# Kernel optimization log

Hardware: AMD Instinct MI355X
Metric: run time of the kernel (lower is better)

## Reference

```python
import jax, jax.numpy as jnp
import numpy as np

NUM_BUCKETS = 320
MAX_DISTANCE = 800


def _layer_norm(x, w, b, eps=1e-5):
    x32 = x.astype(jnp.float32)
    mu = x32.mean(-1, keepdims=True)
    var = x32.var(-1, keepdims=True)
    return ((x32 - mu) / jnp.sqrt(var + eps) * w + b).astype(x.dtype)


def _rel_pos_bucket(rel):
    half = NUM_BUCKETS // 2            # 160
    st = half // 2                     # 80 (small threshold)
    sign = (rel >= 0).astype(jnp.int32)
    ab = jnp.abs(rel)
    is_small = ab < st
    log_ratio = jnp.log(jnp.clip(ab.astype(jnp.float32), 1.0) / st) / np.float32(np.log(MAX_DISTANCE / st))
    log_pos = st + (log_ratio * (half - st)).astype(jnp.int32)  # trunc toward zero like .long()
    log_pos = jnp.minimum(log_pos, half - 1)
    bucket = jnp.where(is_small, ab, log_pos) + sign * half
    return jnp.clip(bucket, 0, NUM_BUCKETS - 1)


def setup_inputs() -> dict:
    key = jax.random.key(0)
    B, T, C, H, FF = 2, 2048, 768, 12, 3072
    D = C // H
    ks = jax.random.split(key, 16)
    s = 0.02
    return {
        "x": jax.random.normal(ks[0], (B, T, C), jnp.float32),
        "ln1_w": jnp.ones((C,), jnp.float32),
        "ln1_b": jnp.zeros((C,), jnp.float32),
        "wq": jax.random.normal(ks[1], (C, C), jnp.float32) * s,
        "bq": jnp.zeros((C,), jnp.float32),
        "wk": jax.random.normal(ks[2], (C, C), jnp.float32) * s,
        "bk": jnp.zeros((C,), jnp.float32),
        "wv": jax.random.normal(ks[3], (C, C), jnp.float32) * s,
        "bv": jnp.zeros((C,), jnp.float32),
        "wo": jax.random.normal(ks[4], (C, C), jnp.float32) * s,
        "bo": jnp.zeros((C,), jnp.float32),
        "ln2_w": jnp.ones((C,), jnp.float32),
        "ln2_b": jnp.zeros((C,), jnp.float32),
        "w1": jax.random.normal(ks[5], (FF, C), jnp.float32) * s,
        "b1": jnp.zeros((FF,), jnp.float32),
        "w2": jax.random.normal(ks[6], (C, FF), jnp.float32) * s,
        "b2": jnp.zeros((C,), jnp.float32),
        "rel_embed": jax.random.normal(ks[7], (NUM_BUCKETS, H), jnp.float32),
        "gate_ur_w": jax.random.normal(ks[8], (H, D), jnp.float32) * 0.01,
        "gate_i_w": jax.random.normal(ks[9], (H, D), jnp.float32) * 0.01,
        "rel_scale": jnp.ones((H,), jnp.float32),
    }


def reference(x, ln1_w, ln1_b, wq, bq, wk, bk, wv, bv, wo, bo,
              ln2_w, ln2_b, w1, b1, w2, b2, rel_embed, gate_ur_w, gate_i_w, rel_scale):
    B, T, C = x.shape
    H = rel_embed.shape[1]
    D = C // H

    residual = x
    h = _layer_norm(x, ln1_w, ln1_b)
    q = (h @ wq.T + bq).reshape(B, T, H, D).transpose(0, 2, 1, 3)  # [B,H,T,D]
    k = (h @ wk.T + bk).reshape(B, T, H, D).transpose(0, 2, 1, 3)
    v = (h @ wv.T + bv).reshape(B, T, H, D).transpose(0, 2, 1, 3)

    attn = jnp.einsum('bhqd,bhkd->bhqk', q, k) * (D ** -0.5)

    # gated relative position bias
    pos = jnp.arange(T)
    rel = pos[None, :] - pos[:, None]                 # [T,T]
    buckets = _rel_pos_bucket(rel)                    # [T,T]
    pe = rel_embed[buckets]                           # [T,T,H]
    pe = jnp.transpose(pe, (2, 0, 1))[None]           # [1,H,T,T]
    g_in = q.mean(axis=2).transpose(0, 2, 1).mean(axis=-1)   # [B,D]
    gate_r = jax.nn.sigmoid(g_in @ gate_ur_w.T)       # [B,H]
    gate_u = jax.nn.sigmoid(g_in @ gate_i_w.T)        # [B,H]
    gate = 1.0 + (gate_u * rel_scale[None, :] * gate_r)[:, :, None, None]
    bias = pe * gate                                  # [B,H,T,T]

    attn = jax.nn.softmax(attn + bias, axis=-1)
    out = jnp.einsum('bhqk,bhkd->bhqd', attn, v).transpose(0, 2, 1, 3).reshape(B, T, C)
    x = residual + out @ wo.T + bo

    residual = x
    h = _layer_norm(x, ln2_w, ln2_b)
    h = jax.nn.gelu(h @ w1.T + b1, approximate=False) @ w2.T + b2
    return residual + h
```

## Files before the change

### kernel.cpp

```cpp
#include <hip/hip_runtime.h>
#include <hip/hip_bf16.h>


#define Tn 2048
#define Cn 768
#define Hn 12
#define Dn 64
#define FFn 3072
#define Mn 4096
#define QKVS 2304

typedef __attribute__((ext_vector_type(8))) short bfrag;
typedef __attribute__((ext_vector_type(8))) unsigned short us8;
typedef __attribute__((ext_vector_type(4))) float f32x4;

__device__ __forceinline__ unsigned short f2bu(float f){
  __hip_bfloat16 h = __float2bfloat16(f);
  return *(unsigned short*)&h;
}
__device__ __forceinline__ float bu2f(unsigned short u){
  union { unsigned int i; float f; } v; v.i = ((unsigned int)u) << 16; return v.f;
}
__device__ __forceinline__ us8 pack8(float4 a, float4 b){
  us8 c;
  c[0]=f2bu(a.x); c[1]=f2bu(a.y); c[2]=f2bu(a.z); c[3]=f2bu(a.w);
  c[4]=f2bu(b.x); c[5]=f2bu(b.y); c[6]=f2bu(b.z); c[7]=f2bu(b.w);
  return c;
}

__device__ __forceinline__ float block_reduce_sum(float v, float* sred){
  #pragma unroll
  for (int off = 32; off > 0; off >>= 1) v += __shfl_down(v, off, 64);
  __syncthreads();
  if ((threadIdx.x & 63) == 0) sred[threadIdx.x >> 6] = v;
  __syncthreads();
  return sred[0] + sred[1] + sred[2] + sred[3];
}
__device__ __forceinline__ float rowsum16(float v){
  v += __shfl_xor(v, 1, 16);
  v += __shfl_xor(v, 2, 16);
  v += __shfl_xor(v, 4, 16);
  v += __shfl_xor(v, 8, 16);
  return v;
}

__global__ __launch_bounds__(256) void cast_all_kernel(
    const float* __restrict__ wq, const float* __restrict__ wk,
    const float* __restrict__ wv, const float* __restrict__ wo,
    const float* __restrict__ w1, const float* __restrict__ w2,
    const float* __restrict__ bq, const float* __restrict__ bk,
    const float* __restrict__ bv,
    unsigned short* __restrict__ Wqkv, unsigned short* __restrict__ Wob,
    unsigned short* __restrict__ W1b, unsigned short* __restrict__ W2b,
    float* __restrict__ bqkv)
{
  const int blk = blockIdx.x;
  if (blk >= 3456){
    const int i = (blk - 3456) * 256 + threadIdx.x;
    bqkv[i] = (i < Cn) ? bq[i] : (i < 2 * Cn) ? bk[i - Cn] : bv[i - 2 * Cn];
    return;
  }
  const float* src; unsigned short* dst; int i;
  if (blk < 288)      { src = wq; dst = Wqkv;               i = blk * 256 + threadIdx.x; }
  else if (blk < 576) { src = wk; dst = Wqkv + Cn * Cn;     i = (blk - 288) * 256 + threadIdx.x; }
  else if (blk < 864) { src = wv; dst = Wqkv + 2 * Cn * Cn; i = (blk - 576) * 256 + threadIdx.x; }
  else if (blk < 1152){ src = wo; dst = Wob;                i = (blk - 864) * 256 + threadIdx.x; }
  else if (blk < 2304){ src = w1; dst = W1b;                i = (blk - 1152) * 256 + threadIdx.x; }
  else                { src = w2; dst = W2b;                i = (blk - 2304) * 256 + threadIdx.x; }
  const float4 a = ((const float4*)src)[i * 2];
  const float4 b = ((const float4*)src)[i * 2 + 1];
  *(us8*)&dst[i * 8] = pack8(a, b);
}

__global__ __launch_bounds__(256) void ln_kernel(const float* __restrict__ xin,
    const float* __restrict__ w, const float* __restrict__ bsh,
    unsigned short* __restrict__ out)
{
  __shared__ float xs[Cn];
  __shared__ float sred[4];
  const size_t base = (size_t)blockIdx.x * Cn;
  float s = 0.f;
  for (int c = threadIdx.x; c < Cn; c += 256){
    float v = xin[base + c];
    xs[c] = v; s += v;
  }
  const float mean = block_reduce_sum(s, sred) * (1.f / Cn);
  float s2 = 0.f;
  for (int c = threadIdx.x; c < Cn; c += 256){
    float d = xs[c] - mean; s2 += d * d;
  }
  const float var = block_reduce_sum(s2, sred) * (1.f / Cn);
  const float rstd = rsqrtf(var + 1e-5f);
  for (int c = threadIdx.x; c < Cn; c += 256)
    out[base + c] = f2bu((xs[c] - mean) * rstd * w[c] + bsh[c]);
}

template<int EPI>
__global__ __launch_bounds__(256) void gemm_mfma_kernel(
    const unsigned short* __restrict__ A, const unsigned short* __restrict__ Bw,
    const float* __restrict__ bias, const float* __restrict__ res,
    void* __restrict__ Cout, int M, int N, int K)
{
  __shared__ __align__(16) unsigned short As[128 * 32];
  __shared__ __align__(16) unsigned short Bs[128 * 32];
  const int tid = threadIdx.x;
  const int lane = tid & 63, w = tid >> 6;
  const int nl = lane & 15, quad = lane >> 4;
  const int wm = w >> 1, wn = w & 1;
  const int bm = blockIdx.y * 128, bn = blockIdx.x * 128;
  const int l4 = lane >> 2, lk = (lane & 3) * 8;

  f32x4 acc[4][4];
  #pragma unroll
  for (int i = 0; i < 4; i++)
    #pragma unroll
    for (int j = 0; j < 4; j++) acc[i][j] = (f32x4){0.f, 0.f, 0.f, 0.f};

  const int c0 = w, c1 = w + 4;
  const unsigned short* A0 = A + (size_t)(bm + c0 * 16 + l4) * K + lk;
  const unsigned short* A1 = A + (size_t)(bm + c1 * 16 + l4) * K + lk;
  const unsigned short* B0 = Bw + (size_t)(bn + c0 * 16 + l4) * K + lk;
  const unsigned short* B1 = Bw + (size_t)(bn + c1 * 16 + l4) * K + lk;

  for (int k0 = 0; k0 < K; k0 += 32){
    __syncthreads();
    __builtin_amdgcn_global_load_lds(
        (const __attribute__((address_space(1))) void*)(A0 + k0),
        (__attribute__((address_space(3))) void*)&As[c0 * 512], 16, 0, 0);
    __builtin_amdgcn_global_load_lds(
        (const __attribute__((address_space(1))) void*)(A1 + k0),
        (__attribute__((address_space(3))) void*)&As[c1 * 512], 16, 0, 0);
    __builtin_amdgcn_global_load_lds(
        (const __attribute__((address_space(1))) void*)(B0 + k0),
        (__attribute__((address_space(3))) void*)&Bs[c0 * 512], 16, 0, 0);
    __builtin_amdgcn_global_load_lds(
        (const __attribute__((address_space(1))) void*)(B1 + k0),
        (__attribute__((address_space(3))) void*)&Bs[c1 * 512], 16, 0, 0);
    __syncthreads();

    bfrag Af[4], Bf[4];
    #pragma unroll
    for (int mt = 0; mt < 4; mt++)
      Af[mt] = *(const bfrag*)&As[(wm * 64 + mt * 16 + nl) * 32 + quad * 8];
    #pragma unroll
    for (int nt = 0; nt < 4; nt++)
      Bf[nt] = *(const bfrag*)&Bs[(wn * 64 + nt * 16 + nl) * 32 + quad * 8];
    #pragma unroll
    for (int mt = 0; mt < 4; mt++)
      #pragma unroll
      for (int nt = 0; nt < 4; nt++)
        acc[mt][nt] = __builtin_amdgcn_mfma_f32_16x16x32_bf16(Af[mt], Bf[nt], acc[mt][nt], 0, 0, 0);
  }

  #pragma unroll
  for (int nt = 0; nt < 4; nt++){
    const int col = bn + wn * 64 + nt * 16 + nl;
    const float bv_ = bias[col];
    #pragma unroll
    for (int mt = 0; mt < 4; mt++){
      const int row0 = bm + wm * 64 + mt * 16 + quad * 4;
      #pragma unroll
      for (int r = 0; r < 4; r++){
        const size_t idx = (size_t)(row0 + r) * N + col;
        const float v = acc[mt][nt][r] + bv_;
        if (EPI == 0){
          ((unsigned short*)Cout)[idx] = f2bu(v);
        } else if (EPI == 1){
          ((float*)Cout)[idx] = v + res[idx];
        } else {
          ((unsigned short*)Cout)[idx] = f2bu(0.5f * v * (1.f + erff(v * 0.70710678118f)));
        }
      }
    }
  }
}

template<int EPI>
__global__ __launch_bounds__(256) void gemm_n64_kernel(
    const unsigned short* __restrict__ A, const unsigned short* __restrict__ Bw,
    const float* __restrict__ bias, const float* __restrict__ res,
    void* __restrict__ Cout, int M, int N, int K)
{
  __shared__ __align__(16) unsigned short As[128 * 32];
  __shared__ __align__(16) unsigned short Bs[64 * 32];
  const int tid = threadIdx.x;
  const int lane = tid & 63, w = tid >> 6;
  const int nl = lane & 15, quad = lane >> 4;
  const int bm = blockIdx.y * 128, bn = blockIdx.x * 64;
  const int l4 = lane >> 2, lk = (lane & 3) * 8;

  f32x4 acc[2][4];
  #pragma unroll
  for (int i = 0; i < 2; i++)
    #pragma unroll
    for (int j = 0; j < 4; j++) acc[i][j] = (f32x4){0.f, 0.f, 0.f, 0.f};

  const unsigned short* A0 = A + (size_t)(bm + w * 16 + l4) * K + lk;
  const unsigned short* A1 = A + (size_t)(bm + (w + 4) * 16 + l4) * K + lk;
  const unsigned short* B0 = Bw + (size_t)(bn + w * 16 + l4) * K + lk;

  for (int k0 = 0; k0 < K; k0 += 32){
    __syncthreads();
    __builtin_amdgcn_global_load_lds(
        (const __attribute__((address_space(1))) void*)(A0 + k0),
        (__attribute__((address_space(3))) void*)&As[w * 512], 16, 0, 0);
    __builtin_amdgcn_global_load_lds(
        (const __attribute__((address_space(1))) void*)(A1 + k0),
        (__attribute__((address_space(3))) void*)&As[(w + 4) * 512], 16, 0, 0);
    __builtin_amdgcn_global_load_lds(
        (const __attribute__((address_space(1))) void*)(B0 + k0),
        (__attribute__((address_space(3))) void*)&Bs[w * 512], 16, 0, 0);
    __syncthreads();

    bfrag Af[2], Bf[4];
    #pragma unroll
    for (int mt = 0; mt < 2; mt++)
      Af[mt] = *(const bfrag*)&As[(w * 32 + mt * 16 + nl) * 32 + quad * 8];
    #pragma unroll
    for (int nt = 0; nt < 4; nt++)
      Bf[nt] = *(const bfrag*)&Bs[(nt * 16 + nl) * 32 + quad * 8];
    #pragma unroll
    for (int mt = 0; mt < 2; mt++)
      #pragma unroll
      for (int nt = 0; nt < 4; nt++)
        acc[mt][nt] = __builtin_amdgcn_mfma_f32_16x16x32_bf16(Af[mt], Bf[nt], acc[mt][nt], 0, 0, 0);
  }

  #pragma unroll
  for (int nt = 0; nt < 4; nt++){
    const int col = bn + nt * 16 + nl;
    const float bv_ = bias[col];
    #pragma unroll
    for (int mt = 0; mt < 2; mt++){
      const int row0 = bm + w * 32 + mt * 16 + quad * 4;
      #pragma unroll
      for (int r = 0; r < 4; r++){
        const size_t idx = (size_t)(row0 + r) * N + col;
        const float v = acc[mt][nt][r] + bv_;
        if (EPI == 1){
          ((float*)Cout)[idx] = v + res[idx];
        } else {
          ((unsigned short*)Cout)[idx] = f2bu(v);
        }
      }
    }
  }
}

__global__ __launch_bounds__(256) void qmean_part_kernel(
    const unsigned short* __restrict__ QKV, float* __restrict__ qpart)
{
  __shared__ float ps[Cn];
  const int b = blockIdx.y, t0 = blockIdx.x * 128;
  const int tid = threadIdx.x;
  float a0 = 0.f, a1 = 0.f, a2 = 0.f;
  for (int r = 0; r < 128; r++){
    const size_t base = (size_t)(b * Tn + t0 + r) * QKVS;
    a0 += bu2f(QKV[base + tid]);
    a1 += bu2f(QKV[base + tid + 256]);
    a2 += bu2f(QKV[base + tid + 512]);
  }
  ps[tid] = a0; ps[tid + 256] = a1; ps[tid + 512] = a2;
  __syncthreads();
  if (tid < Dn){
    float s = 0.f;
    #pragma unroll
    for (int hh = 0; hh < Hn; hh++) s += ps[hh * Dn + tid];
    qpart[(b * 16 + blockIdx.x) * Dn + tid] = s;
  }
}

__global__ __launch_bounds__(64) void gate_kernel(const float* __restrict__ qpart,
    const float* __restrict__ gur, const float* __restrict__ gi,
    const float* __restrict__ rsc, float* __restrict__ gate)
{
  const int b = blockIdx.x / Hn, h = blockIdx.x % Hn;
  const int d = threadIdx.x;
  float s = 0.f;
  #pragma unroll
  for (int blk = 0; blk < 16; blk++) s += qpart[(b * 16 + blk) * Dn + d];
  const float g = s * (1.f / (Hn * Tn));
  float vr = g * gur[h * Dn + d];
  float vu = g * gi[h * Dn + d];
  #pragma unroll
  for (int off = 32; off > 0; off >>= 1){
    vr += __shfl_down(vr, off, 64);
    vu += __shfl_down(vu, off, 64);
  }
  if (d == 0){
    const float gr = 1.f / (1.f + __expf(-vr));
    const float gu = 1.f / (1.f + __expf(-vu));
    gate[blockIdx.x] = 1.f + gu * rsc[h] * gr;
  }
}

__global__ void bias_kernel(const float* __restrict__ rel_embed,
                            float* __restrict__ bias_rel)
{
  const int idx = blockIdx.x * 256 + threadIdx.x;
  if (idx >= 4095) return;
  const int rel = idx - 2047;
  const int ab = rel < 0 ? -rel : rel;
  int bucket;
  if (ab < 80){
    bucket = ab;
  } else {
    const float lr = logf((float)ab * (1.0f / 80.0f)) * (1.0f / 2.3025851f);
    int lp = 80 + (int)(lr * 80.0f);
    bucket = lp < 159 ? lp : 159;
  }
  if (rel >= 0) bucket += 160;
  #pragma unroll
  for (int h = 0; h < Hn; h++)
    bias_rel[h * 4095 + idx] = rel_embed[bucket * Hn + h];
}

__global__ __launch_bounds__(256) void attn_mfma_kernel(
    const unsigned short* __restrict__ QKV, const float* __restrict__ bias_rel,
    const float* __restrict__ gate, unsigned short* __restrict__ O)
{
  __shared__ __align__(16) char smem[9216 * 4 + 1024];
  unsigned short* Qs = (unsigned short*)smem;
  float* bias_blk    = (float*)smem;
  unsigned short* Ks = (unsigned short*)(smem + 9216);
  unsigned short* Vt = (unsigned short*)(smem + 18432);
  unsigned short* Ps = (unsigned short*)(smem + 27648);
  float* lsh         = (float*)(smem + 36864);

  const int qbase = blockIdx.x * 64;
  const int h = blockIdx.y, b = blockIdx.z;
  const int tid = threadIdx.x;
  const float g = gate[b * Hn + h];
  const float* brow = bias_rel + h * 4095 + 1984 - qbase;
  const unsigned short* Q = QKV;
  const unsigned short* K = QKV + Cn;
  const unsigned short* V = QKV + 2 * Cn;

  {
    const int row = tid >> 2, cg = (tid & 3) * 16;
    const us8* qp = (const us8*)(Q + (size_t)(b * Tn + qbase + row) * QKVS + h * Dn + cg);
    *(us8*)&Qs[row * 72 + cg]     = qp[0];
    *(us8*)&Qs[row * 72 + cg + 8] = qp[1];
  }
  __syncthreads();

  const int lane = tid & 63, w = tid >> 6;
  const int nl = lane & 15, quad = lane >> 4;

  bfrag Qa[4][2];
  #pragma unroll
  for (int mt = 0; mt < 4; mt++){
    Qa[mt][0] = *(const bfrag*)&Qs[(mt * 16 + nl) * 72 + quad * 8];
    Qa[mt][1] = *(const bfrag*)&Qs[(mt * 16 + nl) * 72 + 32 + quad * 8];
  }
  __syncthreads();
  for (int j = tid; j < 2112; j += 256) bias_blk[j] = brow[j] * g;

  const int wq = w & 1, wd = w >> 1;
  f32x4 Oa[2][2];
  #pragma unroll
  for (int a = 0; a < 2; a++)
    #pragma unroll
    for (int d0 = 0; d0 < 2; d0++) Oa[a][d0] = (f32x4){0.f, 0.f, 0.f, 0.f};
  float l_acc[4][4];
  #pragma unroll
  for (int mt = 0; mt < 4; mt++)
    #pragma unroll
    for (int r = 0; r < 4; r++) l_acc[mt][r] = 0.f;

  const int skey = tid >> 2, sdg = (tid & 3) * 16;
  const int vkey = tid & 63, vwg = (tid >> 6) * 16;

  for (int kt = 0; kt < 32; kt++){
    const int kbase = kt * 64;
    __syncthreads();
    {
      const us8* kp = (const us8*)(K + (size_t)(b * Tn + kbase + skey) * QKVS + h * Dn + sdg);
      *(us8*)&Ks[skey * 72 + sdg]     = kp[0];
      *(us8*)&Ks[skey * 72 + sdg + 8] = kp[1];
    }
    {
      const us8* vp = (const us8*)(V + (size_t)(b * Tn + kbase + vkey) * QKVS + h * Dn + vwg);
      const us8 a = vp[0], c = vp[1];
      #pragma unroll
      for (int j = 0; j < 8; j++){
        Vt[(vwg + j) * 72 + vkey]     = a[j];
        Vt[(vwg + 8 + j) * 72 + vkey] = c[j];
      }
    }
    __syncthreads();

    const bfrag B0 = *(const bfrag*)&Ks[(w * 16 + nl) * 72 + quad * 8];
    const bfrag B1 = *(const bfrag*)&Ks[(w * 16 + nl) * 72 + 32 + quad * 8];
    #pragma unroll
    for (int mt = 0; mt < 4; mt++){
      f32x4 z = (f32x4){0.f, 0.f, 0.f, 0.f};
      z = __builtin_amdgcn_mfma_f32_16x16x32_bf16(Qa[mt][0], B0, z, 0, 0, 0);
      z = __builtin_amdgcn_mfma_f32_16x16x32_bf16(Qa[mt][1], B1, z, 0, 0, 0);
      const int j0 = kbase + 63 + w * 16 + nl - (mt * 16 + quad * 4);
      const float* bb = &bias_blk[j0];
      #pragma unroll
      for (int r = 0; r < 4; r++){
        const float p = __expf(z[r] * 0.125f + bb[-r]);
        l_acc[mt][r] += p;
        Ps[(mt * 16 + quad * 4 + r) * 72 + w * 16 + nl] = f2bu(p);
      }
    }
    __syncthreads();

    #pragma unroll
    for (int a = 0; a < 2; a++){
      const int mtq = wq * 2 + a;
      const bfrag Pa0 = *(const bfrag*)&Ps[(mtq * 16 + nl) * 72 + quad * 8];
      const bfrag Pa1 = *(const bfrag*)&Ps[(mtq * 16 + nl) * 72 + 32 + quad * 8];
      #pragma unroll
      for (int d0 = 0; d0 < 2; d0++){
        const int dt = wd * 2 + d0;
        const bfrag V0 = *(const bfrag*)&Vt[(dt * 16 + nl) * 72 + quad * 8];
        const bfrag V1 = *(const bfrag*)&Vt[(dt * 16 + nl) * 72 + 32 + quad * 8];
        Oa[a][d0] = __builtin_amdgcn_mfma_f32_16x16x32_bf16(Pa0, V0, Oa[a][d0], 0, 0, 0);
        Oa[a][d0] = __builtin_amdgcn_mfma_f32_16x16x32_bf16(Pa1, V1, Oa[a][d0], 0, 0, 0);
      }
    }
  }

  #pragma unroll
  for (int mt = 0; mt < 4; mt++)
    #pragma unroll
    for (int r = 0; r < 4; r++) l_acc[mt][r] = rowsum16(l_acc[mt][r]);
  if (nl == 0){
    #pragma unroll
    for (int mt = 0; mt < 4; mt++)
      #pragma unroll
      for (int r = 0; r < 4; r++)
        lsh[w * 64 + mt * 16 + quad * 4 + r] = l_acc[mt][r];
  }
  __syncthreads();
  #pragma unroll
  for (int a = 0; a < 2; a++){
    const int qloc0 = (wq * 2 + a) * 16 + quad * 4;
    #pragma unroll
    for (int r = 0; r < 4; r++){
      const int q = qloc0 + r;
      const float linv = 1.f / (lsh[q] + lsh[64 + q] + lsh[128 + q] + lsh[192 + q]);
      unsigned short* orow = O + (size_t)(b * Tn + qbase + q) * Cn + h * Dn;
      #pragma unroll
      for (int d0 = 0; d0 < 2; d0++)
        orow[(wd * 2 + d0) * 16 + nl] = f2bu(Oa[a][d0][r] * linv);
    }
  }
}

extern "C" void kernel_launch(void* const* d_in, const int* in_sizes, int n_in,
                              void* d_out, int out_size, void* d_ws, size_t ws_size,
                              hipStream_t stream)
{
  const float* x     = (const float*)d_in[0];
  const float* ln1_w = (const float*)d_in[1];
  const float* ln1_b = (const float*)d_in[2];
  const float* wq    = (const float*)d_in[3];
  const float* bq    = (const float*)d_in[4];
  const float* wk    = (const float*)d_in[5];
  const float* bk    = (const float*)d_in[6];
  const float* wv    = (const float*)d_in[7];
  const float* bv    = (const float*)d_in[8];
  const float* wo    = (const float*)d_in[9];
  const float* bo    = (const float*)d_in[10];
  const float* ln2_w = (const float*)d_in[11];
  const float* ln2_b = (const float*)d_in[12];
  const float* w1    = (const float*)d_in[13];
  const float* b1    = (const float*)d_in[14];
  const float* w2    = (const float*)d_in[15];
  const float* b2    = (const float*)d_in[16];
  const float* rel_embed = (const float*)d_in[17];
  const float* gur   = (const float*)d_in[18];
  const float* gi    = (const float*)d_in[19];
  const float* rsc   = (const float*)d_in[20];

  char* ws = (char*)d_ws;
  unsigned short* QKV  = (unsigned short*)(ws);
  unsigned short* Ob   = (unsigned short*)(ws + 18874368);
  float*          X2   = (float*)(ws + 25165824);
  unsigned short* Hb   = (unsigned short*)(ws + 37748736);
  unsigned short* Wqkv = (unsigned short*)(ws + 44040192);
  unsigned short* Wob  = (unsigned short*)(ws + 47579136);
  unsigned short* W1b  = (unsigned short*)(ws + 48758784);
  unsigned short* W2b  = (unsigned short*)(ws + 53477376);
  float*          bqkv = (float*)(ws + 58195968);
  float*          bias_rel = (float*)(ws + 58205184);
  float*          qpart = (float*)(ws + 58401744);
  float*          gate  = (float*)(ws + 58409936);
  unsigned short* Fb   = QKV;

  cast_all_kernel<<<3465, 256, 0, stream>>>(wq, wk, wv, wo, w1, w2, bq, bk, bv,
                                            Wqkv, Wob, W1b, W2b, bqkv);
  ln_kernel<<<Mn, 256, 0, stream>>>(x, ln1_w, ln1_b, Hb);
  gemm_mfma_kernel<0><<<dim3(QKVS / 128, Mn / 128), 256, 0, stream>>>(
      Hb, Wqkv, bqkv, nullptr, QKV, Mn, QKVS, Cn);
  qmean_part_kernel<<<dim3(16, 2), 256, 0, stream>>>(QKV, qpart);
  gate_kernel<<<2 * Hn, 64, 0, stream>>>(qpart, gur, gi, rsc, gate);
  bias_kernel<<<16, 256, 0, stream>>>(rel_embed, bias_rel);
  attn_mfma_kernel<<<dim3(Tn / 64, Hn, 2), 256, 0, stream>>>(QKV, bias_rel, gate, Ob);
  gemm_n64_kernel<1><<<dim3(Cn / 64, Mn / 128), 256, 0, stream>>>(
      Ob, Wob, bo, x, X2, Mn, Cn, Cn);
  ln_kernel<<<Mn, 256, 0, stream>>>(X2, ln2_w, ln2_b, Hb);
  gemm_mfma_kernel<2><<<dim3(FFn / 128, Mn / 128), 256, 0, stream>>>(
      Hb, W1b, b1, nullptr, Fb, Mn, FFn, Cn);
  gemm_n64_kernel<1><<<dim3(Cn / 64, Mn / 128), 256, 0, stream>>>(
      Fb, W2b, b2, X2, (float*)d_out, Mn, Cn, FFn);
}
```

Measured before the change: 365.9 us.

## Double-buffer GEMM LDS loads, emit transposed V from QKV GEMM, use exp2 softmax

Both GEMM kernels now use two LDS buffers, so the global-to-LDS load of the next K slice is issued before the MFMAs on the current slice run, overlapping memory latency with compute. The QKV GEMM writes V already transposed into a separate [C, M] buffer, and Q/K go into a narrower 1536-wide buffer. This lets the attention kernel load V tiles with vector loads instead of doing a scalar transpose into LDS. Softmax now uses a hardware exp2, with log2(e) folded into the bias table and the scale. The cost is double the LDS footprint per GEMM block and uncoalesced 8-byte stores in the V-transpose epilogue.

Result: no change. 373.1 us (+2.0%).

```diff
diff --git a/kernel.cpp b/kernel.cpp
--- a/kernel.cpp
+++ b/kernel.cpp
@@ -9,10 +9,15 @@
 #define FFn 3072
 #define Mn 4096
 #define QKVS 2304
+#define LQK 1536
 
 typedef __attribute__((ext_vector_type(8))) short bfrag;
 typedef __attribute__((ext_vector_type(8))) unsigned short us8;
 typedef __attribute__((ext_vector_type(4))) float f32x4;
+
+#define GLDS(gptr, lptr) __builtin_amdgcn_global_load_lds( \
+    (const __attribute__((address_space(1))) void*)(gptr), \
+    (__attribute__((address_space(3))) void*)(lptr), 16, 0, 0)
 
 __device__ __forceinline__ unsigned short f2bu(float f){
   __hip_bfloat16 h = __float2bfloat16(f);
@@ -27,6 +32,7 @@
   c[4]=f2bu(b.x); c[5]=f2bu(b.y); c[6]=f2bu(b.z); c[7]=f2bu(b.w);
   return c;
 }
+__device__ __forceinline__ float fexp2(float x){ return __builtin_amdgcn_exp2f(x); }
 
 __device__ __forceinline__ float block_reduce_sum(float v, float* sred){
   #pragma unroll
@@ -95,14 +101,31 @@
     out[base + c] = f2bu((xs[c] - mean) * rstd * w[c] + bsh[c]);
 }
 
-template<int EPI>
+__device__ __forceinline__ void gemm_step128(const unsigned short* As,
+    const unsigned short* Bs, f32x4 acc[4][4], int wm, int wn, int nl, int quad)
+{
+  bfrag Af[4], Bf[4];
+  #pragma unroll
+  for (int mt = 0; mt < 4; mt++)
+    Af[mt] = *(const bfrag*)&As[(wm * 64 + mt * 16 + nl) * 32 + quad * 8];
+  #pragma unroll
+  for (int nt = 0; nt < 4; nt++)
+    Bf[nt] = *(const bfrag*)&Bs[(wn * 64 + nt * 16 + nl) * 32 + quad * 8];
+  #pragma unroll
+  for (int mt = 0; mt < 4; mt++)
+    #pragma unroll
+    for (int nt = 0; nt < 4; nt++)
+      acc[mt][nt] = __builtin_amdgcn_mfma_f32_16x16x32_bf16(Af[mt], Bf[nt], acc[mt][nt], 0, 0, 0);
+}
+
+template<int EPI, bool TRANSV>
 __global__ __launch_bounds__(256) void gemm_mfma_kernel(
     const unsigned short* __restrict__ A, const unsigned short* __restrict__ Bw,
-    const float* __restrict__ bias, const float* __restrict__ res,
-    void* __restrict__ Cout, int M, int N, int K)
-{
-  __shared__ __align__(16) unsigned short As[128 * 32];
-  __shared__ __align__(16) unsigned short Bs[128 * 32];
+    const float* __restrict__ bias, unsigned short* __restrict__ vt,
+    void* __restrict__ Cout, int M, int N, int K, int ldo)
+{
+  __shared__ __align__(16) unsigned short As[2][128 * 32];
+  __shared__ __align__(16) unsigned short Bs[2][128 * 32];
   const int tid = threadIdx.x;
   const int lane = tid & 63, w = tid >> 6;
   const int nl = lane & 15, quad = lane >> 4;
@@ -122,36 +145,39 @@
   const unsigned short* B0 = Bw + (size_t)(bn + c0 * 16 + l4) * K + lk;
   const unsigned short* B1 = Bw + (size_t)(bn + c1 * 16 + l4) * K + lk;
 
-  for (int k0 = 0; k0 < K; k0 += 32){
-    __syncthreads();
-    __builtin_amdgcn_global_load_lds(
-        (const __attribute__((address_space(1))) void*)(A0 + k0),
-        (__attribute__((address_space(3))) void*)&As[c0 * 512], 16, 0, 0);
-    __builtin_amdgcn_global_load_lds(
-        (const __attribute__((address_space(1))) void*)(A1 + k0),
-        (__attribute__((address_space(3))) void*)&As[c1 * 512], 16, 0, 0);
-    __builtin_amdgcn_global_load_lds(
-        (const __attribute__((address_space(1))) void*)(B0 + k0),
-        (__attribute__((address_space(3))) void*)&Bs[c0 * 512], 16, 0, 0);
-    __builtin_amdgcn_global_load_lds(
-        (const __attribute__((address_space(1))) void*)(B1 + k0),
-        (__attribute__((address_space(3))) void*)&Bs[c1 * 512], 16, 0, 0);
-    __syncthreads();
-
-    bfrag Af[4], Bf[4];
-    #pragma unroll
-    for (int mt = 0; mt < 4; mt++)
-      Af[mt] = *(const bfrag*)&As[(wm * 64 + mt * 16 + nl) * 32 + quad * 8];
-    #pragma unroll
-    for (int nt = 0; nt < 4; nt++)
-      Bf[nt] = *(const bfrag*)&Bs[(wn * 64 + nt * 16 + nl) * 32 + quad * 8];
-    #pragma unroll
-    for (int mt = 0; mt < 4; mt++)
-      #pragma unroll
-      for (int nt = 0; nt < 4; nt++)
-        acc[mt][nt] = __builtin_amdgcn_mfma_f32_16x16x32_bf16(Af[mt], Bf[nt], acc[mt][nt], 0, 0, 0);
-  }
-
+  GLDS(A0, &As[0][c0 * 512]); GLDS(A1, &As[0][c1 * 512]);
+  GLDS(B0, &Bs[0][c0 * 512]); GLDS(B1, &Bs[0][c1 * 512]);
+
+  for (int k0 = 0; k0 < K; k0 += 64){
+    __syncthreads();
+    GLDS(A0 + k0 + 32, &As[1][c0 * 512]); GLDS(A1 + k0 + 32, &As[1][c1 * 512]);
+    GLDS(B0 + k0 + 32, &Bs[1][c0 * 512]); GLDS(B1 + k0 + 32, &Bs[1][c1 * 512]);
+    gemm_step128(As[0], Bs[0], acc, wm, wn, nl, quad);
+    __syncthreads();
+    if (k0 + 64 < K){
+      GLDS(A0 + k0 + 64, &As[0][c0 * 512]); GLDS(A1 + k0 + 64, &As[0][c1 * 512]);
+      GLDS(B0 + k0 + 64, &Bs[0][c0 * 512]); GLDS(B1 + k0 + 64, &Bs[0][c1 * 512]);
+    }
+    gemm_step128(As[1], Bs[1], acc, wm, wn, nl, quad);
+  }
+
+  if (TRANSV && bn >= 1536){
+    #pragma unroll
+    for (int nt = 0; nt < 4; nt++){
+      const int col = bn + wn * 64 + nt * 16 + nl;
+      const float bv_ = bias[col];
+      const int vcol = col - 1536;
+      #pragma unroll
+      for (int mt = 0; mt < 4; mt++){
+        const int row0 = bm + wm * 64 + mt * 16 + quad * 4;
+        unsigned short pk[4];
+        #pragma unroll
+        for (int r = 0; r < 4; r++) pk[r] = f2bu(acc[mt][nt][r] + bv_);
+        *(uint2*)&vt[(size_t)vcol * Mn + row0] = *(uint2*)pk;
+      }
+    }
+    return;
+  }
   #pragma unroll
   for (int nt = 0; nt < 4; nt++){
     const int col = bn + wn * 64 + nt * 16 + nl;
@@ -161,28 +187,25 @@
       const int row0 = bm + wm * 64 + mt * 16 + quad * 4;
       #pragma unroll
       for (int r = 0; r < 4; r++){
-        const size_t idx = (size_t)(row0 + r) * N + col;
+        const size_t idx = (size_t)(row0 + r) * ldo + col;
         const float v = acc[mt][nt][r] + bv_;
-        if (EPI == 0){
+        if (EPI == 2){
+          ((unsigned short*)Cout)[idx] = f2bu(0.5f * v * (1.f + erff(v * 0.70710678118f)));
+        } else {
           ((unsigned short*)Cout)[idx] = f2bu(v);
-        } else if (EPI == 1){
-          ((float*)Cout)[idx] = v + res[idx];
-        } else {
-          ((unsigned short*)Cout)[idx] = f2bu(0.5f * v * (1.f + erff(v * 0.70710678118f)));
         }
       }
     }
   }
 }
 
-template<int EPI>
 __global__ __launch_bounds__(256) void gemm_n64_kernel(
     const unsigned short* __restrict__ A, const unsigned short* __restrict__ Bw,
     const float* __restrict__ bias, const float* __restrict__ res,
-    void* __restrict__ Cout, int M, int N, int K)
-{
-  __shared__ __align__(16) unsigned short As[128 * 32];
-  __shared__ __align__(16) unsigned short Bs[64 * 32];
+    float* __restrict__ Cout, int M, int N, int K)
+{
+  __shared__ __align__(16) unsigned short As[2][128 * 32];
+  __shared__ __align__(16) unsigned short Bs[2][64 * 32];
   const int tid = threadIdx.x;
   const int lane = tid & 63, w = tid >> 6;
   const int nl = lane & 15, quad = lane >> 4;
@@ -199,31 +222,46 @@
   const unsigned short* A1 = A + (size_t)(bm + (w + 4) * 16 + l4) * K + lk;
   const unsigned short* B0 = Bw + (size_t)(bn + w * 16 + l4) * K + lk;
 
-  for (int k0 = 0; k0 < K; k0 += 32){
-    __syncthreads();
-    __builtin_amdgcn_global_load_lds(
-        (const __attribute__((address_space(1))) void*)(A0 + k0),
-        (__attribute__((address_space(3))) void*)&As[w * 512], 16, 0, 0);
-    __builtin_amdgcn_global_load_lds(
-        (const __attribute__((address_space(1))) void*)(A1 + k0),
-        (__attribute__((address_space(3))) void*)&As[(w + 4) * 512], 16, 0, 0);
-    __builtin_amdgcn_global_load_lds(
-        (const __attribute__((address_space(1))) void*)(B0 + k0),
-        (__attribute__((address_space(3))) void*)&Bs[w * 512], 16, 0, 0);
-    __syncthreads();
-
-    bfrag Af[2], Bf[4];
-    #pragma unroll
-    for (int mt = 0; mt < 2; mt++)
-      Af[mt] = *(const bfrag*)&As[(w * 32 + mt * 16 + nl) * 32 + quad * 8];
-    #pragma unroll
-    for (int nt = 0; nt < 4; nt++)
-      Bf[nt] = *(const bfrag*)&Bs[(nt * 16 + nl) * 32 + quad * 8];
-    #pragma unroll
-    for (int mt = 0; mt < 2; mt++)
+  GLDS(A0, &As[0][w * 512]); GLDS(A1, &As[0][(w + 4) * 512]);
+  GLDS(B0, &Bs[0][w * 512]);
+
+  for (int k0 = 0; k0 < K; k0 += 64){
+    __syncthreads();
+    GLDS(A0 + k0 + 32, &As[1][w * 512]); GLDS(A1 + k0 + 32, &As[1][(w + 4) * 512]);
+    GLDS(B0 + k0 + 32, &Bs[1][w * 512]);
+    {
+      bfrag Af[2], Bf[4];
+      #pragma unroll
+      for (int mt = 0; mt < 2; mt++)
+        Af[mt] = *(const bfrag*)&As[0][(w * 32 + mt * 16 + nl) * 32 + quad * 8];
       #pragma unroll
       for (int nt = 0; nt < 4; nt++)
-        acc[mt][nt] = __builtin_amdgcn_mfma_f32_16x16x32_bf16(Af[mt], Bf[nt], acc[mt][nt], 0, 0, 0);
+        Bf[nt] = *(const bfrag*)&Bs[0][(nt * 16 + nl) * 32 + quad * 8];
+      #pragma unroll
+      for (int mt = 0; mt < 2; mt++)
+        #pragma unroll
+        for (int nt = 0; nt < 4; nt++)
+          acc[mt][nt] = __builtin_amdgcn_mfma_f32_16x16x32_bf16(Af[mt], Bf[nt], acc[mt][nt], 0, 0, 0);
+    }
+    __syncthreads();
+    if (k0 + 64 < K){
+      GLDS(A0 + k0 + 64, &As[0][w * 512]); GLDS(A1 + k0 + 64, &As[0][(w + 4) * 512]);
+      GLDS(B0 + k0 + 64, &Bs[0][w * 512]);
+    }
+    {
+      bfrag Af[2], Bf[4];
+      #pragma unroll
+      for (int mt = 0; mt < 2; mt++)
+        Af[mt] = *(const bfrag*)&As[1][(w * 32 + mt * 16 + nl) * 32 + quad * 8];
+      #pragma unroll
+      for (int nt = 0; nt < 4; nt++)
+        Bf[nt] = *(const bfrag*)&Bs[1][(nt * 16 + nl) * 32 + quad * 8];
+      #pragma unroll
+      for (int mt = 0; mt < 2; mt++)
+        #pragma unroll
+        for (int nt = 0; nt < 4; nt++)
+          acc[mt][nt] = __builtin_amdgcn_mfma_f32_16x16x32_bf16(Af[mt], Bf[nt], acc[mt][nt], 0, 0, 0);
+    }
   }
 
   #pragma unroll
@@ -236,29 +274,24 @@
       #pragma unroll
       for (int r = 0; r < 4; r++){
         const size_t idx = (size_t)(row0 + r) * N + col;
-        const float v = acc[mt][nt][r] + bv_;
-        if (EPI == 1){
-          ((float*)Cout)[idx] = v + res[idx];
-        } else {
-          ((unsigned short*)Cout)[idx] = f2bu(v);
-        }
+        Cout[idx] = acc[mt][nt][r] + bv_ + res[idx];
       }
     }
   }
 }
 
 __global__ __launch_bounds__(256) void qmean_part_kernel(
-    const unsigned short* __restrict__ QKV, float* __restrict__ qpart)
+    const unsigned short* __restrict__ QKVqk, float* __restrict__ qpart)
 {
   __shared__ float ps[Cn];
   const int b = blockIdx.y, t0 = blockIdx.x * 128;
   const int tid = threadIdx.x;
   float a0 = 0.f, a1 = 0.f, a2 = 0.f;
   for (int r = 0; r < 128; r++){
-    const size_t base = (size_t)(b * Tn + t0 + r) * QKVS;
-    a0 += bu2f(QKV[base + tid]);
-    a1 += bu2f(QKV[base + tid + 256]);
-    a2 += bu2f(QKV[base + tid + 512]);
+    const size_t base = (size_t)(b * Tn + t0 + r) * LQK;
+    a0 += bu2f(QKVqk[base + tid]);
+    a1 += bu2f(QKVqk[base + tid + 256]);
+    a2 += bu2f(QKVqk[base + tid + 512]);
   }
   ps[tid] = a0; ps[tid + 256] = a1; ps[tid + 512] = a2;
   __syncthreads();
@@ -312,12 +345,13 @@
   if (rel >= 0) bucket += 160;
   #pragma unroll
   for (int h = 0; h < Hn; h++)
-    bias_rel[h * 4095 + idx] = rel_embed[bucket * Hn + h];
+    bias_rel[h * 4095 + idx] = rel_embed[bucket * Hn + h] * 1.44269504089f;
 }
 
 __global__ __launch_bounds__(256) void attn_mfma_kernel(
-    const unsigned short* __restrict__ QKV, const float* __restrict__ bias_rel,
-    const float* __restrict__ gate, unsigned short* __restrict__ O)
+    const unsigned short* __restrict__ QKVqk, const unsigned short* __restrict__ VT,
+    const float* __restrict__ bias_rel, const float* __restrict__ gate,
+    unsigned short* __restrict__ O)
 {
   __shared__ __align__(16) char smem[9216 * 4 + 1024];
   unsigned short* Qs = (unsigned short*)smem;
@@ -332,13 +366,12 @@
   const int tid = threadIdx.x;
   const float g = gate[b * Hn + h];
   const float* brow = bias_rel + h * 4095 + 1984 - qbase;
-  const unsigned short* Q = QKV;
-  const unsigned short* K = QKV + Cn;
-  const unsigned short* V = QKV + 2 * Cn;
+  const unsigned short* Q = QKVqk;
+  const unsigned short* K = QKVqk + Cn;
 
   {
     const int row = tid >> 2, cg = (tid & 3) * 16;
-    const us8* qp = (const us8*)(Q + (size_t)(b * Tn + qbase + row) * QKVS + h * Dn + cg);
+    const us8* qp = (const us8*)(Q + (size_t)(b * Tn + qbase + row) * LQK + h * Dn + cg);
     *(us8*)&Qs[row * 72 + cg]     = qp[0];
     *(us8*)&Qs[row * 72 + cg + 8] = qp[1];
   }
@@ -354,7 +387,7 @@
     Qa[mt][1] = *(const bfrag*)&Qs[(mt * 16 + nl) * 72 + 32 + quad * 8];
   }
   __syncthreads();
-  for (int j = tid; j < 2112; j += 256) bias_blk[j] = brow[j] * g;
+  for (int j = tid; j < 2111; j += 256) bias_blk[j] = brow[j] * g;
 
   const int wq = w & 1, wd = w >> 1;
   f32x4 Oa[2][2];
@@ -369,45 +402,49 @@
     for (int r = 0; r < 4; r++) l_acc[mt][r] = 0.f;
 
   const int skey = tid >> 2, sdg = (tid & 3) * 16;
-  const int vkey = tid & 63, vwg = (tid >> 6) * 16;
+  const int vd = tid >> 3, vk8 = (tid & 7) * 8;
+  const unsigned short* vtg = VT + (size_t)(h * Dn) * Mn + (size_t)b * Tn;
 
   for (int kt = 0; kt < 32; kt++){
     const int kbase = kt * 64;
     __syncthreads();
     {
-      const us8* kp = (const us8*)(K + (size_t)(b * Tn + kbase + skey) * QKVS + h * Dn + sdg);
+      const us8* kp = (const us8*)(K + (size_t)(b * Tn + kbase + skey) * LQK + h * Dn + sdg);
       *(us8*)&Ks[skey * 72 + sdg]     = kp[0];
       *(us8*)&Ks[skey * 72 + sdg + 8] = kp[1];
     }
     {
-      const us8* vp = (const us8*)(V + (size_t)(b * Tn + kbase + vkey) * QKVS + h * Dn + vwg);
-      const us8 a = vp[0], c = vp[1];
-      #pragma unroll
-      for (int j = 0; j < 8; j++){
-        Vt[(vwg + j) * 72 + vkey]     = a[j];
-        Vt[(vwg + 8 + j) * 72 + vkey] = c[j];
-      }
+      const us8 v0 = *(const us8*)&vtg[(size_t)vd * Mn + kbase + vk8];
+      const us8 v1 = *(const us8*)&vtg[(size_t)(32 + vd) * Mn + kbase + vk8];
+      *(us8*)&Vt[vd * 72 + vk8]        = v0;
+      *(us8*)&Vt[(32 + vd) * 72 + vk8] = v1;
     }
     __syncthreads();
 
     const bfrag B0 = *(const bfrag*)&Ks[(w * 16 + nl) * 72 + quad * 8];
     const bfrag B1 = *(const bfrag*)&Ks[(w * 16 + nl) * 72 + 32 + quad * 8];
+    const int bofs = kbase + 63 + w * 16 + nl - quad * 4;
     #pragma unroll
     for (int mt = 0; mt < 4; mt++){
       f32x4 z = (f32x4){0.f, 0.f, 0.f, 0.f};
       z = __builtin_amdgcn_mfma_f32_16x16x32_bf16(Qa[mt][0], B0, z, 0, 0, 0);
       z = __builtin_amdgcn_mfma_f32_16x16x32_bf16(Qa[mt][1], B1, z, 0, 0, 0);
-      const int j0 = kbase + 63 + w * 16 + nl - (mt * 16 + quad * 4);
-      const float* bb = &bias_blk[j0];
       #pragma unroll
       for (int r = 0; r < 4; r++){
-        const float p = __expf(z[r] * 0.125f + bb[-r]);
+        const float p = fexp2(z[r] * 0.18033688f + bias_blk[bofs - mt * 16 - r]);
         l_acc[mt][r] += p;
         Ps[(mt * 16 + quad * 4 + r) * 72 + w * 16 + nl] = f2bu(p);
       }
     }
     __syncthreads();
 
+    bfrag Vf[2][2];
+    #pragma unroll
+    for (int d0 = 0; d0 < 2; d0++){
+      const int dt = wd * 2 + d0;
+      Vf[d0][0] = *(const bfrag*)&Vt[(dt * 16 + nl) * 72 + quad * 8];
+      Vf[d0][1] = *(const bfrag*)&Vt[(dt * 16 + nl) * 72 + 32 + quad * 8];
+    }
     #pragma unroll
     for (int a = 0; a < 2; a++){
       const int mtq = wq * 2 + a;
@@ -415,11 +452,8 @@
       const bfrag Pa1 = *(const bfrag*)&Ps[(mtq * 16 + nl) * 72 + 32 + quad * 8];
       #pragma unroll
       for (int d0 = 0; d0 < 2; d0++){
-        const int dt = wd * 2 + d0;
-        const bfrag V0 = *(const bfrag*)&Vt[(dt * 16 + nl) * 72 + quad * 8];
-        const bfrag V1 = *(const bfrag*)&Vt[(dt * 16 + nl) * 72 + 32 + quad * 8];
-        Oa[a][d0] = __builtin_amdgcn_mfma_f32_16x16x32_bf16(Pa0, V0, Oa[a][d0], 0, 0, 0);
-        Oa[a][d0] = __builtin_amdgcn_mfma_f32_16x16x32_bf16(Pa1, V1, Oa[a][d0], 0, 0, 0);
+        Oa[a][d0] = __builtin_amdgcn_mfma_f32_16x16x32_bf16(Pa0, Vf[d0][0], Oa[a][d0], 0, 0, 0);
+        Oa[a][d0] = __builtin_amdgcn_mfma_f32_16x16x32_bf16(Pa1, Vf[d0][1], Oa[a][d0], 0, 0, 0);
       }
     }
   }
@@ -478,34 +512,35 @@
   const float* rsc   = (const float*)d_in[20];
 
   char* ws = (char*)d_ws;
-  unsigned short* QKV  = (unsigned short*)(ws);
-  unsigned short* Ob   = (unsigned short*)(ws + 18874368);
-  float*          X2   = (float*)(ws + 25165824);
-  unsigned short* Hb   = (unsigned short*)(ws + 37748736);
-  unsigned short* Wqkv = (unsigned short*)(ws + 44040192);
-  unsigned short* Wob  = (unsigned short*)(ws + 47579136);
-  unsigned short* W1b  = (unsigned short*)(ws + 48758784);
-  unsigned short* W2b  = (unsigned short*)(ws + 53477376);
-  float*          bqkv = (float*)(ws + 58195968);
+  unsigned short* QKVqk = (unsigned short*)(ws);
+  unsigned short* VT    = (unsigned short*)(ws + 12582912);
+  unsigned short* Ob    = (unsigned short*)(ws + 18874368);
+  float*          X2    = (float*)(ws + 25165824);
+  unsigned short* Hb    = (unsigned short*)(ws + 37748736);
+  unsigned short* Wqkv  = (unsigned short*)(ws + 44040192);
+  unsigned short* Wob   = (unsigned short*)(ws + 47579136);
+  unsigned short* W1b   = (unsigned short*)(ws + 48758784);
+  unsigned short* W2b   = (unsigned short*)(ws + 53477376);
+  float*          bqkv  = (float*)(ws + 58195968);
   float*          bias_rel = (float*)(ws + 58205184);
   float*          qpart = (float*)(ws + 58401744);
   float*          gate  = (float*)(ws + 58409936);
-  unsigned short* Fb   = QKV;
+  unsigned short* Fb    = (unsigned short*)(ws);
 
   cast_all_kernel<<<3465, 256, 0, stream>>>(wq, wk, wv, wo, w1, w2, bq, bk, bv,
                                             Wqkv, Wob, W1b, W2b, bqkv);
   ln_kernel<<<Mn, 256, 0, stream>>>(x, ln1_w, ln1_b, Hb);
-  gemm_mfma_kernel<0><<<dim3(QKVS / 128, Mn / 128), 256, 0, stream>>>(
-      Hb, Wqkv, bqkv, nullptr, QKV, Mn, QKVS, Cn);
-  qmean_part_kernel<<<dim3(16, 2), 256, 0, stream>>>(QKV, qpart);
+  gemm_mfma_kernel<0, true><<<dim3(QKVS / 128, Mn / 128), 256, 0, stream>>>(
+      Hb, Wqkv, bqkv, VT, QKVqk, Mn, QKVS, Cn, LQK);
+  qmean_part_kernel<<<dim3(16, 2), 256, 0, stream>>>(QKVqk, qpart);
   gate_kernel<<<2 * Hn, 64, 0, stream>>>(qpart, gur, gi, rsc, gate);
   bias_kernel<<<16, 256, 0, stream>>>(rel_embed, bias_rel);
-  attn_mfma_kernel<<<dim3(Tn / 64, Hn, 2), 256, 0, stream>>>(QKV, bias_rel, gate, Ob);
-  gemm_n64_kernel<1><<<dim3(Cn / 64, Mn / 128), 256, 0, stream>>>(
+  attn_mfma_kernel<<<dim3(Tn / 64, Hn, 2), 256, 0, stream>>>(QKVqk, VT, bias_rel, gate, Ob);
+  gemm_n64_kernel<<<dim3(Cn / 64, Mn / 128), 256, 0, stream>>>(
       Ob, Wob, bo, x, X2, Mn, Cn, Cn);
   ln_kernel<<<Mn, 256, 0, stream>>>(X2, ln2_w, ln2_b, Hb);
-  gemm_mfma_kernel<2><<<dim3(FFn / 128, Mn / 128), 256, 0, stream>>>(
-      Hb, W1b, b1, nullptr, Fb, Mn, FFn, Cn);
-  gemm_n64_kernel<1><<<dim3(Cn / 64, Mn / 128), 256, 0, stream>>>(
+  gemm_mfma_kernel<2, false><<<dim3(FFn / 128, Mn / 128), 256, 0, stream>>>(
+      Hb, W1b, b1, nullptr, Fb, Mn, FFn, Cn, FFn);
+  gemm_n64_kernel<<<dim3(Cn / 64, Mn / 128), 256, 0, stream>>>(
       Fb, W2b, b2, X2, (float*)d_out, Mn, Cn, FFn);
 }
```
